# Performance work log

Hardware: AMD Instinct MI355X
Metric: run time of the kernel (lower is better)

The kernel has to match this reference:

```python
import jax, jax.numpy as jnp
import numpy as np

EPS = 1e-5

def _bn(x, g, b, m, v):
    # eval-mode batchnorm over channel axis 1 of NCHW
    scale = g * jax.lax.rsqrt(v + EPS)
    return x * scale[None, :, None, None] + (b - m * scale)[None, :, None, None]

def _dwconv3x3(x, w):
    # x: [N,C,H,W], w: [C,1,3,3] depthwise, stride 1, pad 1
    C = x.shape[1]
    return jax.lax.conv_general_dilated(
        x, w, window_strides=(1, 1), padding=((1, 1), (1, 1)),
        dimension_numbers=('NCHW', 'OIHW', 'NCHW'), feature_group_count=C)

def setup_inputs() -> dict:
    key = jax.random.key(0)
    ks = jax.random.split(key, 16)
    N, C, H, W = 32, 96, 56, 56
    Hd = 576  # hidden_dim = round(96 * 6)
    inp = {}
    inp['x'] = jax.random.normal(ks[0], (N, C, H, W), jnp.float32)
    inp['w1'] = jax.random.normal(ks[1], (Hd, C), jnp.float32) * 0.05
    inp['g1'] = jax.random.uniform(ks[2], (Hd,), jnp.float32, 0.5, 1.5)
    inp['b1'] = jax.random.normal(ks[3], (Hd,), jnp.float32) * 0.1
    inp['m1'] = jax.random.normal(ks[4], (Hd,), jnp.float32) * 0.1
    inp['v1'] = jax.random.uniform(ks[5], (Hd,), jnp.float32, 0.5, 1.5)
    inp['wdw'] = jax.random.normal(ks[6], (Hd, 1, 3, 3), jnp.float32) * 0.1
    inp['gdw'] = jax.random.uniform(ks[7], (Hd,), jnp.float32, 0.5, 1.5)
    inp['bdw'] = jax.random.normal(ks[8], (Hd,), jnp.float32) * 0.1
    inp['mdw'] = jax.random.normal(ks[9], (Hd,), jnp.float32) * 0.1
    inp['vdw'] = jax.random.uniform(ks[10], (Hd,), jnp.float32, 0.5, 1.5)
    inp['w2'] = jax.random.normal(ks[11], (C, Hd), jnp.float32) * 0.05
    inp['g2'] = jax.random.uniform(ks[12], (C,), jnp.float32, 0.5, 1.5)
    inp['b2'] = jax.random.normal(ks[13], (C,), jnp.float32) * 0.1
    inp['m2'] = jax.random.normal(ks[14], (C,), jnp.float32) * 0.1
    inp['v2'] = jax.random.uniform(ks[15], (C,), jnp.float32, 0.5, 1.5)
    return inp

def reference(x, w1, g1, b1, m1, v1, wdw, gdw, bdw, mdw, vdw, w2, g2, b2, m2, v2):
    # expand 1x1 conv (as GEMM) + BN + ReLU
    h = jnp.einsum('oc,bchw->bohw', w1, x)
    h = jax.nn.relu(_bn(h, g1, b1, m1, v1))
    # depthwise 3x3 + BN + ReLU
    h = _dwconv3x3(h, wdw)
    h = jax.nn.relu(_bn(h, gdw, bdw, mdw, vdw))
    # project 1x1 conv + BN (no ReLU)
    out = jnp.einsum('oc,bchw->bohw', w2, h)
    out = _bn(out, g2, b2, m2, v2)
    # residual (stride==1, inp==oup)
    return x + out
```

## Files before the change

### kernel.cpp

```cpp
#include <hip/hip_runtime.h>
#include <hip/hip_bf16.h>

typedef __attribute__((ext_vector_type(8))) short bf16x8;
typedef __attribute__((ext_vector_type(4))) float f32x4;
typedef unsigned short u16;
typedef unsigned int u32;

#define EPS 1e-5f
#define CIN 96
#define HD 576
#define HW 3136
#define NB 32

#define XTS   104
#define HC_OFF 0
#define HCS   338
#define H2_OFF (64 * HCS * 2)
#define H2S   72
#define SMEM_BYTES (H2_OFF + 224 * H2S * 2)

__device__ __forceinline__ u16 f2bf(float f) {
  u32 u = __builtin_bit_cast(u32, f);
  u32 r = u + 0x7fffu + ((u >> 16) & 1u);
  return (u16)(r >> 16);
}
__device__ __forceinline__ float bf2f(u16 h) {
  return __builtin_bit_cast(float, (u32)h << 16);
}

__global__ __launch_bounds__(256) void prep_kernel(
    const float* __restrict__ w1, const float* __restrict__ w2,
    const float* __restrict__ g1, const float* __restrict__ b1,
    const float* __restrict__ m1, const float* __restrict__ v1,
    const float* __restrict__ gdw, const float* __restrict__ bdw,
    const float* __restrict__ mdw, const float* __restrict__ vdw,
    const float* __restrict__ g2, const float* __restrict__ b2,
    const float* __restrict__ m2, const float* __restrict__ v2,
    u16* __restrict__ w1b, u16* __restrict__ w2b, float* __restrict__ bn)
{
  int i = blockIdx.x * 256 + threadIdx.x;
  if (i < HD * CIN) {
    w1b[i] = f2bf(w1[i]);
    w2b[i] = f2bf(w2[i]);
  }
  if (i < HD) {
    float s = g1[i] * rsqrtf(v1[i] + EPS);
    bn[i] = s;
    bn[HD + i] = b1[i] - m1[i] * s;
    float sd = gdw[i] * rsqrtf(vdw[i] + EPS);
    bn[2 * HD + i] = sd;
    bn[3 * HD + i] = bdw[i] - mdw[i] * sd;
  }
  if (i < CIN) {
    float s2 = g2[i] * rsqrtf(v2[i] + EPS);
    bn[4 * HD + i] = s2;
    bn[4 * HD + CIN + i] = b2[i] - m2[i] * s2;
  }
}

__global__ __launch_bounds__(448, 2) void fused_kernel(
    const float* __restrict__ x, const u16* __restrict__ w1b,
    const u16* __restrict__ w2b, const float* __restrict__ wdw,
    const float* __restrict__ bnp, float* __restrict__ out)
{
  extern __shared__ __align__(16) char smem[];
  u16* Xt  = (u16*)(smem);
  u16* Hc  = (u16*)(smem + HC_OFF);
  u16* H2c = (u16*)(smem + H2_OFF);

  const int tid = threadIdx.x;
  const int r0  = blockIdx.x * 4;
  const int b   = blockIdx.y;
  const int l   = tid & 63;
  const int w   = tid >> 6;
  const int lr  = l & 15;
  const int kq  = l >> 4;
  const int kb  = kq * 8;

  const float* xb = x + (size_t)b * CIN * HW;
  const int pbase = (r0 - 1) * 56;
#pragma unroll
  for (int it = 0; it < 9; ++it) {
    int i = it * 448 + tid;
    int px = i % 336;
    int g  = i / 336;
    int gpx = pbase + px;
    gpx = gpx < 0 ? 0 : (gpx > HW - 1 ? HW - 1 : gpx);
    const float* xp = xb + (size_t)(g * 8) * HW + gpx;
    bf16x8 pk;
#pragma unroll
    for (int j = 0; j < 8; ++j) pk[j] = (short)f2bf(xp[(size_t)j * HW]);
    *(bf16x8*)&Xt[px * XTS + g * 8] = pk;
  }
  __syncthreads();

  bf16x8 xf[3][3];
#pragma unroll
  for (int t = 0; t < 3; ++t)
#pragma unroll
    for (int ks = 0; ks < 3; ++ks)
      xf[t][ks] = *(const bf16x8*)&Xt[((w * 3 + t) * 16 + lr) * XTS + ks * 32 + kb];
  __syncthreads();

  const int chl_dw = tid & 63;
  f32x4 pacc[2][6] = {};

  for (int kc = 0; kc < 9; ++kc) {
    const int ch0 = kc * 64;

    const int gch_dw = ch0 + chl_dw;
    float wk[9];
#pragma unroll
    for (int k = 0; k < 9; ++k) wk[k] = wdw[gch_dw * 9 + k];
    const float sdw = bnp[2 * HD + gch_dw], hdw = bnp[3 * HD + gch_dw];

    bf16x8 af[4][3];
#pragma unroll
    for (int mt = 0; mt < 4; ++mt)
#pragma unroll
      for (int ks = 0; ks < 3; ++ks)
        af[mt][ks] = *(const bf16x8*)&w1b[(size_t)(ch0 + mt * 16 + lr) * CIN + ks * 32 + kb];

    f32x4 bsc[4], bsh[4];
#pragma unroll
    for (int mt = 0; mt < 4; ++mt) {
      bsc[mt] = *(const f32x4*)&bnp[ch0 + mt * 16 + kq * 4];
      bsh[mt] = *(const f32x4*)&bnp[HD + ch0 + mt * 16 + kq * 4];
    }

#pragma unroll
    for (int t = 0; t < 3; ++t) {
      f32x4 ea[4] = {};
#pragma unroll
      for (int ks = 0; ks < 3; ++ks) {
        ea[0] = __builtin_amdgcn_mfma_f32_16x16x32_bf16(af[0][ks], xf[t][ks], ea[0], 0, 0, 0);
        ea[1] = __builtin_amdgcn_mfma_f32_16x16x32_bf16(af[1][ks], xf[t][ks], ea[1], 0, 0, 0);
        ea[2] = __builtin_amdgcn_mfma_f32_16x16x32_bf16(af[2][ks], xf[t][ks], ea[2], 0, 0, 0);
        ea[3] = __builtin_amdgcn_mfma_f32_16x16x32_bf16(af[3][ks], xf[t][ks], ea[3], 0, 0, 0);
      }
      const int hpx = (w * 3 + t) * 16 + lr;
#pragma unroll
      for (int mt = 0; mt < 4; ++mt)
#pragma unroll
        for (int i = 0; i < 4; ++i) {
          int chl = mt * 16 + kq * 4 + i;
          float v = fmaxf(ea[mt][i] * bsc[mt][i] + bsh[mt][i], 0.f);
          Hc[chl * HCS + hpx] = f2bf(v);
        }
    }
    __syncthreads();

#pragma unroll
    for (int it = 0; it < 2; ++it) {
      int cg = (tid >> 6) + it * 7;
      int c0 = cg * 4;

      float win[6][8];
#pragma unroll
      for (int hr = 0; hr < 6; ++hr) {
        int grow = r0 - 1 + hr;
        bool rv = (grow >= 0) && (grow < 56);
        const u16* rp = &Hc[chl_dw * HCS + hr * 56];
#pragma unroll
        for (int k2 = 0; k2 < 4; ++k2) {
          int cb = c0 - 2 + k2 * 2;
          u32 pr = (rv && cb >= 0) ? *(const u32*)(rp + cb) : 0u;
          win[hr][k2 * 2]     = bf2f((u16)pr);
          win[hr][k2 * 2 + 1] = bf2f((u16)(pr >> 16));
        }
        if (c0 + 4 >= 56) win[hr][6] = 0.f;
      }
#pragma unroll
      for (int orr = 0; orr < 4; ++orr) {
        float a4[4] = {0.f, 0.f, 0.f, 0.f};
#pragma unroll
        for (int dy = 0; dy < 3; ++dy)
#pragma unroll
          for (int j = 0; j < 4; ++j)
#pragma unroll
            for (int dx = 0; dx < 3; ++dx)
              a4[j] += wk[dy * 3 + dx] * win[orr + dy][j + dx + 1];
#pragma unroll
        for (int j = 0; j < 4; ++j) {
          float v = fmaxf(a4[j] * sdw + hdw, 0.f);
          H2c[(orr * 56 + c0 + j) * H2S + chl_dw] = f2bf(v);
        }
      }
    }
    __syncthreads();

    bf16x8 pa[6][2];
#pragma unroll
    for (int mt = 0; mt < 6; ++mt)
#pragma unroll
      for (int ks = 0; ks < 2; ++ks)
        pa[mt][ks] = *(const bf16x8*)&w2b[(size_t)(mt * 16 + lr) * HD + ch0 + ks * 32 + kb];
#pragma unroll
    for (int ntl = 0; ntl < 2; ++ntl) {
      int pt = w * 2 + ntl;
      bf16x8 pb[2];
#pragma unroll
      for (int ks = 0; ks < 2; ++ks)
        pb[ks] = *(const bf16x8*)&H2c[(pt * 16 + lr) * H2S + ks * 32 + kb];
#pragma unroll
      for (int ks = 0; ks < 2; ++ks)
#pragma unroll
        for (int mt = 0; mt < 6; ++mt)
          pacc[ntl][mt] = __builtin_amdgcn_mfma_f32_16x16x32_bf16(pa[mt][ks], pb[ks], pacc[ntl][mt], 0, 0, 0);
    }
  }

  const float* xr = x   + (size_t)b * CIN * HW + r0 * 56;
  float*       ob = out + (size_t)b * CIN * HW + r0 * 56;
#pragma unroll
  for (int mt = 0; mt < 6; ++mt) {
    f32x4 s2 = *(const f32x4*)&bnp[4 * HD + mt * 16 + kq * 4];
    f32x4 h2 = *(const f32x4*)&bnp[4 * HD + CIN + mt * 16 + kq * 4];
#pragma unroll
    for (int ntl = 0; ntl < 2; ++ntl) {
      int opx = (w * 2 + ntl) * 16 + lr;
#pragma unroll
      for (int i = 0; i < 4; ++i) {
        int c = mt * 16 + kq * 4 + i;
        float v = pacc[ntl][mt][i] * s2[i] + h2[i];
        size_t idx = (size_t)c * HW + opx;
        ob[idx] = v + xr[idx];
      }
    }
  }
}

extern "C" void kernel_launch(void* const* d_in, const int* in_sizes, int n_in,
                              void* d_out, int out_size, void* d_ws, size_t ws_size,
                              hipStream_t stream) {
  const float* x   = (const float*)d_in[0];
  const float* w1  = (const float*)d_in[1];
  const float* g1  = (const float*)d_in[2];
  const float* b1  = (const float*)d_in[3];
  const float* m1  = (const float*)d_in[4];
  const float* v1  = (const float*)d_in[5];
  const float* wdw = (const float*)d_in[6];
  const float* gdw = (const float*)d_in[7];
  const float* bdw = (const float*)d_in[8];
  const float* mdw = (const float*)d_in[9];
  const float* vdw = (const float*)d_in[10];
  const float* w2  = (const float*)d_in[11];
  const float* g2  = (const float*)d_in[12];
  const float* b2  = (const float*)d_in[13];
  const float* m2  = (const float*)d_in[14];
  const float* v2  = (const float*)d_in[15];
  float* out = (float*)d_out;

  char* ws = (char*)d_ws;
  u16*   w1b = (u16*)ws;
  u16*   w2b = (u16*)(ws + 2 * (size_t)HD * CIN);
  float* bnp = (float*)(ws + 4 * (size_t)HD * CIN);

  (void)hipFuncSetAttribute((const void*)fused_kernel,
                            hipFuncAttributeMaxDynamicSharedMemorySize, SMEM_BYTES);

  prep_kernel<<<dim3((HD * CIN + 255) / 256), 256, 0, stream>>>(
      w1, w2, g1, b1, m1, v1, gdw, bdw, mdw, vdw, g2, b2, m2, v2, w1b, w2b, bnp);

  fused_kernel<<<dim3(14, NB), 448, SMEM_BYTES, stream>>>(x, w1b, w2b, wdw, bnp, out);
}
```

Baseline: 255.2 us.

## Halve hidden-channel chunk to shrink LDS and load x directly into registers

Processes the 576 hidden channels in 32-channel chunks instead of 64, so each of the 18 iterations does half the expand and project MFMA work. The depthwise stage is remapped so all 448 threads cover 32 channels × 14 column groups in one pass. The x tile is loaded straight from global into MFMA B fragments, which removes the LDS staging buffer and two barriers. LDS use drops to about 40 KB and the dynamic-smem attribute call is removed. In exchange the number of per-chunk barriers and weight reloads doubles.

```diff
diff --git a/kernel.cpp b/kernel.cpp
--- a/kernel.cpp
+++ b/kernel.cpp
@@ -12,11 +12,10 @@
 #define HW 3136
 #define NB 32
 
-#define XTS   104
+#define HCS   338
 #define HC_OFF 0
-#define HCS   338
-#define H2_OFF (64 * HCS * 2)
-#define H2S   72
+#define H2_OFF 21632
+#define H2S   40
 #define SMEM_BYTES (H2_OFF + 224 * H2S * 2)
 
 __device__ __forceinline__ u16 f2bf(float f) {
@@ -64,7 +63,6 @@
     const float* __restrict__ bnp, float* __restrict__ out)
 {
   extern __shared__ __align__(16) char smem[];
-  u16* Xt  = (u16*)(smem);
   u16* Hc  = (u16*)(smem + HC_OFF);
   u16* H2c = (u16*)(smem + H2_OFF);
 
@@ -79,34 +77,28 @@
 
   const float* xb = x + (size_t)b * CIN * HW;
   const int pbase = (r0 - 1) * 56;
-#pragma unroll
-  for (int it = 0; it < 9; ++it) {
-    int i = it * 448 + tid;
-    int px = i % 336;
-    int g  = i / 336;
-    int gpx = pbase + px;
+  bf16x8 xf[3][3];
+#pragma unroll
+  for (int t = 0; t < 3; ++t) {
+    int gpx = pbase + (w * 3 + t) * 16 + lr;
     gpx = gpx < 0 ? 0 : (gpx > HW - 1 ? HW - 1 : gpx);
-    const float* xp = xb + (size_t)(g * 8) * HW + gpx;
-    bf16x8 pk;
-#pragma unroll
-    for (int j = 0; j < 8; ++j) pk[j] = (short)f2bf(xp[(size_t)j * HW]);
-    *(bf16x8*)&Xt[px * XTS + g * 8] = pk;
-  }
-  __syncthreads();
-
-  bf16x8 xf[3][3];
-#pragma unroll
-  for (int t = 0; t < 3; ++t)
-#pragma unroll
-    for (int ks = 0; ks < 3; ++ks)
-      xf[t][ks] = *(const bf16x8*)&Xt[((w * 3 + t) * 16 + lr) * XTS + ks * 32 + kb];
-  __syncthreads();
-
-  const int chl_dw = tid & 63;
+    const float* xp = xb + gpx;
+#pragma unroll
+    for (int ks = 0; ks < 3; ++ks) {
+      bf16x8 pk;
+#pragma unroll
+      for (int j = 0; j < 8; ++j)
+        pk[j] = (short)f2bf(xp[(size_t)(ks * 32 + kq * 8 + j) * HW]);
+      xf[t][ks] = pk;
+    }
+  }
+
+  const int chl_dw = tid & 31;
+  const int cg_dw  = tid >> 5;
   f32x4 pacc[2][6] = {};
 
-  for (int kc = 0; kc < 9; ++kc) {
-    const int ch0 = kc * 64;
+  for (int kc = 0; kc < 18; ++kc) {
+    const int ch0 = kc * 32;
 
     const int gch_dw = ch0 + chl_dw;
     float wk[9];
@@ -114,33 +106,31 @@
     for (int k = 0; k < 9; ++k) wk[k] = wdw[gch_dw * 9 + k];
     const float sdw = bnp[2 * HD + gch_dw], hdw = bnp[3 * HD + gch_dw];
 
-    bf16x8 af[4][3];
-#pragma unroll
-    for (int mt = 0; mt < 4; ++mt)
+    bf16x8 af[2][3];
+#pragma unroll
+    for (int mt = 0; mt < 2; ++mt)
 #pragma unroll
       for (int ks = 0; ks < 3; ++ks)
         af[mt][ks] = *(const bf16x8*)&w1b[(size_t)(ch0 + mt * 16 + lr) * CIN + ks * 32 + kb];
 
-    f32x4 bsc[4], bsh[4];
-#pragma unroll
-    for (int mt = 0; mt < 4; ++mt) {
+    f32x4 bsc[2], bsh[2];
+#pragma unroll
+    for (int mt = 0; mt < 2; ++mt) {
       bsc[mt] = *(const f32x4*)&bnp[ch0 + mt * 16 + kq * 4];
       bsh[mt] = *(const f32x4*)&bnp[HD + ch0 + mt * 16 + kq * 4];
     }
 
 #pragma unroll
     for (int t = 0; t < 3; ++t) {
-      f32x4 ea[4] = {};
+      f32x4 ea[2] = {};
 #pragma unroll
       for (int ks = 0; ks < 3; ++ks) {
         ea[0] = __builtin_amdgcn_mfma_f32_16x16x32_bf16(af[0][ks], xf[t][ks], ea[0], 0, 0, 0);
         ea[1] = __builtin_amdgcn_mfma_f32_16x16x32_bf16(af[1][ks], xf[t][ks], ea[1], 0, 0, 0);
-        ea[2] = __builtin_amdgcn_mfma_f32_16x16x32_bf16(af[2][ks], xf[t][ks], ea[2], 0, 0, 0);
-        ea[3] = __builtin_amdgcn_mfma_f32_16x16x32_bf16(af[3][ks], xf[t][ks], ea[3], 0, 0, 0);
       }
       const int hpx = (w * 3 + t) * 16 + lr;
 #pragma unroll
-      for (int mt = 0; mt < 4; ++mt)
+      for (int mt = 0; mt < 2; ++mt)
 #pragma unroll
         for (int i = 0; i < 4; ++i) {
           int chl = mt * 16 + kq * 4 + i;
@@ -150,11 +140,8 @@
     }
     __syncthreads();
 
-#pragma unroll
-    for (int it = 0; it < 2; ++it) {
-      int cg = (tid >> 6) + it * 7;
-      int c0 = cg * 4;
-
+    {
+      const int c0 = cg_dw * 4;
       float win[6][8];
 #pragma unroll
       for (int hr = 0; hr < 6; ++hr) {
@@ -189,24 +176,17 @@
     }
     __syncthreads();
 
-    bf16x8 pa[6][2];
+    bf16x8 pa[6];
 #pragma unroll
     for (int mt = 0; mt < 6; ++mt)
-#pragma unroll
-      for (int ks = 0; ks < 2; ++ks)
-        pa[mt][ks] = *(const bf16x8*)&w2b[(size_t)(mt * 16 + lr) * HD + ch0 + ks * 32 + kb];
+      pa[mt] = *(const bf16x8*)&w2b[(size_t)(mt * 16 + lr) * HD + ch0 + kb];
 #pragma unroll
     for (int ntl = 0; ntl < 2; ++ntl) {
       int pt = w * 2 + ntl;
-      bf16x8 pb[2];
-#pragma unroll
-      for (int ks = 0; ks < 2; ++ks)
-        pb[ks] = *(const bf16x8*)&H2c[(pt * 16 + lr) * H2S + ks * 32 + kb];
-#pragma unroll
-      for (int ks = 0; ks < 2; ++ks)
-#pragma unroll
-        for (int mt = 0; mt < 6; ++mt)
-          pacc[ntl][mt] = __builtin_amdgcn_mfma_f32_16x16x32_bf16(pa[mt][ks], pb[ks], pacc[ntl][mt], 0, 0, 0);
+      bf16x8 pb = *(const bf16x8*)&H2c[(pt * 16 + lr) * H2S + kb];
+#pragma unroll
+      for (int mt = 0; mt < 6; ++mt)
+        pacc[ntl][mt] = __builtin_amdgcn_mfma_f32_16x16x32_bf16(pa[mt], pb, pacc[ntl][mt], 0, 0, 0);
     }
   }
 
@@ -256,9 +236,6 @@
   u16*   w2b = (u16*)(ws + 2 * (size_t)HD * CIN);
   float* bnp = (float*)(ws + 4 * (size_t)HD * CIN);
 
-  (void)hipFuncSetAttribute((const void*)fused_kernel,
-                            hipFuncAttributeMaxDynamicSharedMemorySize, SMEM_BYTES);
-
   prep_kernel<<<dim3((HD * CIN + 255) / 256), 256, 0, stream>>>(
       w1, w2, g1, b1, m1, v1, gdw, bdw, mdw, vdw, g2, b2, m2, v2, w1b, w2b, bnp);
 
```

Measured after the change: 259.5 us. No clear change (+1.7%).
